# Optimization experiments

Hardware: AMD Instinct MI355X
Metric: run time of the kernel (lower is better)

The kernel has to match this reference:

```python
import jax, jax.numpy as jnp
import numpy as np
import math

B, S, E = 4, 2048, 1024


def setup_inputs() -> dict:
    key = jax.random.key(0)
    ks = jax.random.split(key, 9)
    x = jax.random.normal(ks[0], (B, S, E), dtype=jnp.float32)
    # causal boolean mask, broadcast over batch: True = keep
    mask = jnp.broadcast_to(jnp.tril(jnp.ones((S, S), dtype=bool)), (B, S, S))
    sc = 1.0 / math.sqrt(E)
    Wq = jax.random.normal(ks[1], (E, E), dtype=jnp.float32) * sc
    bq = jnp.zeros((E,), dtype=jnp.float32)
    Wk = jax.random.normal(ks[2], (E, E), dtype=jnp.float32) * sc
    bk = jnp.zeros((E,), dtype=jnp.float32)
    Wv = jax.random.normal(ks[3], (E, E), dtype=jnp.float32) * sc
    bv = jnp.zeros((E,), dtype=jnp.float32)
    gamma = jnp.ones((E,), dtype=jnp.float32)
    beta = jnp.zeros((E,), dtype=jnp.float32)
    return {"x": x, "mask": mask, "Wq": Wq, "bq": bq, "Wk": Wk, "bk": bk,
            "Wv": Wv, "bv": bv, "gamma": gamma, "beta": beta}


def reference(x, mask, Wq, bq, Wk, bk, Wv, bv, gamma, beta):
    E_ = x.shape[-1]
    q = jnp.einsum('bse,fe->bsf', x, Wq) + bq
    k = jnp.einsum('bse,fe->bsf', x, Wk) + bk
    v = jnp.einsum('bse,fe->bsf', x, Wv) + bv
    scores = jnp.einsum('bqe,bke->bqk', q, k) / jnp.sqrt(jnp.float32(E_))
    scores = jnp.where(mask, scores, -jnp.inf)
    probs = jax.nn.softmax(scores, axis=-1)
    attn = jnp.einsum('bqk,bke->bqe', probs, v)
    y = attn + x
    # LayerNorm over last dim, eps matches torch default 1e-5
    mu = jnp.mean(y, axis=-1, keepdims=True)
    var = jnp.mean(jnp.square(y - mu), axis=-1, keepdims=True)
    return (y - mu) / jnp.sqrt(var + 1e-5) * gamma + beta
```

## Files before the change

kernel.cpp:

```cpp
#include <hip/hip_runtime.h>
#include <hip/hip_bf16.h>
#include <stdint.h>

#define B_ 4
#define S_ 2048
#define E_ 1024
#define BS_ (B_*S_)

using bf16x8 = __attribute__((ext_vector_type(8))) __bf16;
using f32x4  = __attribute__((ext_vector_type(4))) float;

__constant__ int pv_mt[24] = {7,8,9,10,11,12,13,14,15,15,14,6,13,5,12,4,11,3,10,2,9,1,8,0};
__constant__ int pv_ck[24] = {0,0,0,0,0,0,0,0,0, 1, 1,0, 1,0, 1,0, 1,0, 1,0, 1,0, 1,0};

__device__ __forceinline__ unsigned short f2bf(float f) {
  unsigned int u = __float_as_uint(f);
  u += 0x7fffu + ((u >> 16) & 1u);
  return (unsigned short)(u >> 16);
}
__device__ __forceinline__ float bf2f(unsigned short h) {
  return __uint_as_float(((unsigned int)h) << 16);
}

__device__ __forceinline__ void gld16(const unsigned short* g, unsigned short* l) {
  __builtin_amdgcn_global_load_lds((__attribute__((address_space(1))) void*)(void*)g,
                                   (__attribute__((address_space(3))) void*)l, 16, 0, 0);
}

__global__ __launch_bounds__(256) void prep_all(
    const float* __restrict__ x,
    const float* __restrict__ Wq, const float* __restrict__ Wk, const float* __restrict__ Wv,
    const float* __restrict__ bq, const float* __restrict__ bk, const float* __restrict__ bv,
    unsigned short* __restrict__ xb, unsigned short* __restrict__ Wb, float* __restrict__ bb,
    float* __restrict__ lz) {
  const int i = blockIdx.x * 256 + threadIdx.x;
  const int nx4 = BS_ * E_ / 4, nw4 = E_ * E_ / 4;
  if (i < nx4) {
    const float4 v = ((const float4*)x)[i];
    ushort4 o;
    o.x = f2bf(v.x); o.y = f2bf(v.y); o.z = f2bf(v.z); o.w = f2bf(v.w);
    ((ushort4*)xb)[i] = o;
  } else if (i < nx4 + 3 * nw4) {
    const int j = i - nx4;
    const int m = j / nw4, jj = j - m * nw4;
    const float* src = (m == 0) ? Wq : (m == 1) ? Wk : Wv;
    const float4 v = ((const float4*)src)[jj];
    ushort4 o;
    o.x = f2bf(v.x); o.y = f2bf(v.y); o.z = f2bf(v.z); o.w = f2bf(v.w);
    ((ushort4*)Wb)[j] = o;
  } else {
    const int j = i - nx4 - 3 * nw4;
    if (j < 3 * E_) bb[j] = (j < E_) ? bq[j] : (j < 2 * E_) ? bk[j - E_] : bv[j - 2 * E_];
    else { const int k = j - 3 * E_; if (k < BS_) lz[k] = 0.f; }
  }
}

template<int EPI>
__device__ __forceinline__ void gemm_body(
    const unsigned short* __restrict__ A, const unsigned short* __restrict__ Bm,
    float* __restrict__ Cf,
    unsigned short* __restrict__ Cb, unsigned short* __restrict__ VtOut,
    const float* __restrict__ bias,
    int K, int lda, int ldb, int ldc,
    long sA, long sB, long sC, float scale)
{
  constexpr int BM = 128, BN = 128, BK = 64;
  __shared__ __align__(16) unsigned short As[BM * BK];
  __shared__ __align__(16) unsigned short Bs[BN * BK];

  int mt, nt, ck = 0, bz;
  if (EPI == 1) {
    const int sig = (blockIdx.x & 7) * 68 + (blockIdx.x >> 3);
    bz = sig / 136;
    const int rem = sig - bz * 136;
    const int M = (rem >= 78) ? 3 : (rem >= 36) ? 2 : (rem >= 10) ? 1 : 0;
    const int cumM = (M == 3) ? 78 : (M == 2) ? 36 : (M == 1) ? 10 : 0;
    const int inner = rem - cumM;
    if (inner < 16 * M) {
      const int N = inner >> 4, t2 = inner & 15;
      mt = 4 * M + (t2 >> 2); nt = 4 * N + (t2 & 3);
    } else {
      const int t2 = inner - 16 * M;
      const int ml = (t2 >= 6) ? 3 : (t2 >= 3) ? 2 : (t2 >= 1) ? 1 : 0;
      const int nl = t2 - (ml * (ml + 1)) / 2;
      mt = 4 * M + ml; nt = 4 * M + nl;
    }
  } else if (EPI == 2) {
    mt = pv_mt[blockIdx.y]; ck = pv_ck[blockIdx.y]; nt = blockIdx.x; bz = blockIdx.z;
  } else {
    const int nwg = gridDim.x * gridDim.y;
    const int bid = blockIdx.y * gridDim.x + blockIdx.x;
    const int swz = (bid & 7) * (nwg >> 3) + (bid >> 3);
    mt = swz / gridDim.x; nt = swz - mt * gridDim.x; bz = blockIdx.z;
  }
  A  += sA * bz;
  Bm += sB * bz;
  const int m0 = mt * BM, n0 = nt * BN;
  const int k0s  = (EPI == 2 && ck) ? 1024 : 0;
  const int kend = (EPI == 2) ? (ck ? m0 + BM : min(1024, m0 + BM)) : K;

  const int t = threadIdx.x;
  const int lane = t & 63, wave = t >> 6;
  const int wr = wave >> 1, wc = wave & 1;
  const int q = lane >> 4, r = lane & 15;

  const int srow   = lane >> 3;
  const int schunk = (lane & 7) ^ srow;
  const long ga0 = (long)(m0 + wave * 32 + srow) * lda + schunk * 8;
  const long gb0 = (long)(n0 + wave * 32 + srow) * ldb + schunk * 8;

  f32x4 acc[4][4] = {};

  for (int k0 = k0s; k0 < kend; k0 += BK) {
#pragma unroll
    for (int s = 0; s < 4; ++s) {
      gld16(A  + ga0 + (long)s * 8 * lda + k0, &As[(wave * 32 + s * 8) * 64]);
      gld16(Bm + gb0 + (long)s * 8 * ldb + k0, &Bs[(wave * 32 + s * 8) * 64]);
    }
    __syncthreads();
#pragma unroll
    for (int kk = 0; kk < BK; kk += 32) {
      bf16x8 af[4], bfr[4];
      const int cq = (kk >> 3) + q;
#pragma unroll
      for (int i = 0; i < 4; ++i) {
        const int row = wr * 64 + i * 16 + r;
        af[i] = *(const bf16x8*)&As[(row * 8 + (cq ^ (r & 7))) * 8];
      }
#pragma unroll
      for (int j = 0; j < 4; ++j) {
        const int row = wc * 64 + j * 16 + r;
        bfr[j] = *(const bf16x8*)&Bs[(row * 8 + (cq ^ (r & 7))) * 8];
      }
#pragma unroll
      for (int i = 0; i < 4; ++i)
#pragma unroll
        for (int j = 0; j < 4; ++j)
          acc[i][j] = __builtin_amdgcn_mfma_f32_16x16x32_bf16(af[i], bfr[j], acc[i][j], 0, 0, 0);
    }
    __syncthreads();
  }

  if (EPI == 0) {
    if (n0 < 2 * E_) {
#pragma unroll
    for (int i = 0; i < 4; ++i)
#pragma unroll
      for (int j = 0; j < 4; ++j) {
        const int col = n0 + wc * 64 + j * 16 + r;
        const float bia = bias[col];
#pragma unroll
        for (int e = 0; e < 4; ++e) {
          const int rowg = m0 + wr * 64 + i * 16 + q * 4 + e;
          Cb[(long)rowg * ldc + col] = f2bf(acc[i][j][e] + bia);
        }
      }
    } else {
      unsigned short* scr = As + wave * 2048;
      const int bb = m0 >> 11;
      const int sbase = (m0 & (S_ - 1)) + wr * 64;
#pragma unroll
      for (int j = 0; j < 4; ++j) {
        const int e_base = n0 - 2 * E_ + wc * 64 + j * 16;
        const float bj = bias[n0 + wc * 64 + j * 16 + r];
#pragma unroll
        for (int i = 0; i < 4; ++i) {
          const int c = 2 * i + (q >> 1);
          const int slot = c ^ (r & 7);
          ushort4 o;
          o.x = f2bf(acc[i][j][0] + bj);
          o.y = f2bf(acc[i][j][1] + bj);
          o.z = f2bf(acc[i][j][2] + bj);
          o.w = f2bf(acc[i][j][3] + bj);
          *(ushort4*)&scr[r * 72 + slot * 8 + (q & 1) * 4] = o;
        }
#pragma unroll
        for (int it = 0; it < 2; ++it) {
          const int er = it * 8 + (lane >> 3);
          const int w = lane & 7;
          const bf16x8 vv = *(const bf16x8*)&scr[er * 72 + w * 8];
          const int so = (w ^ (er & 7)) * 8;
          *(bf16x8*)&VtOut[((long)bb * E_ + e_base + er) * S_ + sbase + so] = vv;
        }
      }
    }
  } else if (EPI == 1) {
    Cb += sC * bz;
    float* lv = Cf + (long)bz * S_;
#pragma unroll
    for (int i = 0; i < 4; ++i) {
      float rs[4] = {0.f, 0.f, 0.f, 0.f};
#pragma unroll
      for (int j = 0; j < 4; ++j) {
        const int col = n0 + wc * 64 + j * 16 + r;
#pragma unroll
        for (int e = 0; e < 4; ++e) {
          const int rowg = m0 + wr * 64 + i * 16 + q * 4 + e;
          float p = 0.f;
          if (col <= rowg) p = __expf(fminf(acc[i][j][e] * scale, 60.f));
          Cb[(long)rowg * ldc + col] = f2bf(p);
          rs[e] += p;
        }
      }
#pragma unroll
      for (int e = 0; e < 4; ++e) {
        float s = rs[e];
        s += __shfl_xor(s, 1); s += __shfl_xor(s, 2);
        s += __shfl_xor(s, 4); s += __shfl_xor(s, 8);
        if (r == 0) atomicAdd(&lv[m0 + wr * 64 + i * 16 + q * 4 + e], s);
      }
    }
  } else {
    const float* lv = Cf + (long)bz * S_;
    unsigned short* dst = (ck ? VtOut : Cb) + sC * bz;
#pragma unroll
    for (int i = 0; i < 4; ++i) {
      const int rb = m0 + wr * 64 + i * 16 + q * 4;
      const float4 l4 = *(const float4*)&lv[rb];
      const float r0 = 1.f / l4.x, r1 = 1.f / l4.y, r2 = 1.f / l4.z, r3 = 1.f / l4.w;
#pragma unroll
      for (int j = 0; j < 4; ++j) {
        const int col = n0 + wc * 64 + j * 16 + r;
        dst[(long)(rb + 0) * ldc + col] = f2bf(acc[i][j][0] * r0);
        dst[(long)(rb + 1) * ldc + col] = f2bf(acc[i][j][1] * r1);
        dst[(long)(rb + 2) * ldc + col] = f2bf(acc[i][j][2] * r2);
        dst[(long)(rb + 3) * ldc + col] = f2bf(acc[i][j][3] * r3);
      }
    }
  }
}

__global__ __launch_bounds__(256, 4) void gemm_qkv(
    const unsigned short* A, const unsigned short* Bm, float* Cf,
    unsigned short* Cb, unsigned short* VtOut, const float* bias,
    int K, int lda, int ldb, int ldc, long sA, long sB, long sC, float scale) {
  gemm_body<0>(A, Bm, Cf, Cb, VtOut, bias, K, lda, ldb, ldc, sA, sB, sC, scale);
}
__global__ __launch_bounds__(256, 4) void gemm_sc(
    const unsigned short* A, const unsigned short* Bm, float* Cf,
    unsigned short* Cb, unsigned short* VtOut, const float* bias,
    int K, int lda, int ldb, int ldc, long sA, long sB, long sC, float scale) {
  gemm_body<1>(A, Bm, Cf, Cb, VtOut, bias, K, lda, ldb, ldc, sA, sB, sC, scale);
}
__global__ __launch_bounds__(256, 4) void gemm_pv(
    const unsigned short* A, const unsigned short* Bm, float* Cf,
    unsigned short* Cb, unsigned short* VtOut, const float* bias,
    int K, int lda, int ldb, int ldc, long sA, long sB, long sC, float scale) {
  gemm_body<2>(A, Bm, Cf, Cb, VtOut, bias, K, lda, ldb, ldc, sA, sB, sC, scale);
}

__global__ __launch_bounds__(256) void residual_ln(
    const unsigned short* __restrict__ attn, const unsigned short* __restrict__ attn2,
    const unsigned short* __restrict__ xb,
    const float* __restrict__ gamma, const float* __restrict__ beta,
    float* __restrict__ out) {
  __shared__ float rs[4], rs2[4];
  const long row = blockIdx.x;
  const int t = threadIdx.x;
  const int lane = t & 63, wave = t >> 6;
  const ushort4 a  = ((const ushort4*)(attn + row * E_))[t];
  const ushort4 xv = ((const ushort4*)(xb + row * E_))[t];
  ushort4 b2 = make_ushort4(0, 0, 0, 0);
  if ((row & (S_ - 1)) >= 1024) b2 = ((const ushort4*)(attn2 + row * E_))[t];
  const float y0 = bf2f(a.x) + bf2f(b2.x) + bf2f(xv.x);
  const float y1 = bf2f(a.y) + bf2f(b2.y) + bf2f(xv.y);
  const float y2 = bf2f(a.z) + bf2f(b2.z) + bf2f(xv.z);
  const float y3 = bf2f(a.w) + bf2f(b2.w) + bf2f(xv.w);
  float s  = y0 + y1 + y2 + y3;
  float s2 = y0 * y0 + y1 * y1 + y2 * y2 + y3 * y3;
#pragma unroll
  for (int o = 32; o; o >>= 1) { s += __shfl_xor(s, o); s2 += __shfl_xor(s2, o); }
  if (lane == 0) { rs[wave] = s; rs2[wave] = s2; }
  __syncthreads();
  s  = rs[0] + rs[1] + rs[2] + rs[3];
  s2 = rs2[0] + rs2[1] + rs2[2] + rs2[3];
  const float mu  = s * (1.0f / E_);
  const float var = s2 * (1.0f / E_) - mu * mu;
  const float inv = rsqrtf(var + 1e-5f);
  const float4 g  = ((const float4*)gamma)[t];
  const float4 be = ((const float4*)beta)[t];
  float4 o;
  o.x = (y0 - mu) * inv * g.x + be.x;
  o.y = (y1 - mu) * inv * g.y + be.y;
  o.z = (y2 - mu) * inv * g.z + be.z;
  o.w = (y3 - mu) * inv * g.w + be.w;
  ((float4*)(out + row * E_))[t] = o;
}

extern "C" void kernel_launch(void* const* d_in, const int* in_sizes, int n_in,
                              void* d_out, int out_size, void* d_ws, size_t ws_size,
                              hipStream_t stream) {
  const float* x  = (const float*)d_in[0];
  const float* Wq = (const float*)d_in[2];
  const float* bq = (const float*)d_in[3];
  const float* Wk = (const float*)d_in[4];
  const float* bk = (const float*)d_in[5];
  const float* Wv = (const float*)d_in[6];
  const float* bv = (const float*)d_in[7];
  const float* gamma = (const float*)d_in[8];
  const float* beta  = (const float*)d_in[9];
  float* out = (float*)d_out;

  char* ws = (char*)d_ws;
  size_t off = 0;
  auto alloc = [&](size_t bytes) { char* p = ws + off; off += (bytes + 255) & ~(size_t)255; return p; };
  unsigned short* xb    = (unsigned short*)alloc((size_t)BS_ * E_ * 2);
  unsigned short* Wqkvb = (unsigned short*)alloc((size_t)3 * E_ * E_ * 2);
  float*          bqkv  = (float*)alloc((size_t)3 * E_ * 4);
  unsigned short* Cqkv  = (unsigned short*)alloc((size_t)BS_ * 2 * E_ * 2);
  unsigned short* Vt    = (unsigned short*)alloc((size_t)BS_ * E_ * 2);
  unsigned short* Sc    = (unsigned short*)alloc((size_t)B_ * S_ * S_ * 2);
  float*          lrow  = (float*)alloc((size_t)BS_ * 4);
  unsigned short* attn  = (unsigned short*)Cqkv;
  unsigned short* attn2 = (unsigned short*)Cqkv + (size_t)BS_ * E_;

  const int nprep = BS_ * E_ / 4 + 3 * E_ * E_ / 4 + 3 * E_ + BS_;
  prep_all<<<dim3((nprep + 255) / 256), 256, 0, stream>>>(x, Wq, Wk, Wv, bq, bk, bv,
                                                          xb, Wqkvb, bqkv, lrow);

  dim3 g1(3 * E_ / 128, BS_ / 128, 1);
  gemm_qkv<<<g1, 256, 0, stream>>>(xb, Wqkvb, nullptr, Cqkv, Vt, bqkv,
                                   E_, E_, E_, 2 * E_, 0, 0, 0, 1.f);

  gemm_sc<<<dim3(544), 256, 0, stream>>>(Cqkv, Cqkv + E_, lrow, Sc, nullptr, nullptr,
                                         E_, 2 * E_, 2 * E_, S_,
                                         (long)S_ * 2 * E_, (long)S_ * 2 * E_, (long)S_ * S_,
                                         0.03125f);

  dim3 g3(E_ / 128, 24, B_);
  gemm_pv<<<g3, 256, 0, stream>>>(Sc, Vt, lrow, attn, attn2, nullptr,
                                  S_, S_, S_, E_,
                                  (long)S_ * S_, (long)S_ * E_, (long)S_ * E_, 1.f);

  residual_ln<<<dim3(BS_), 256, 0, stream>>>(attn, attn2, xb, gamma, beta, out);
}
```

Measured before the change: 270.3 us.

## Replace causal score GEMM with 64x128 tile kernel over lower-triangular tiles

Replaces the 128x128 causal score GEMM, with its grouped triangular tile mapping, by a dedicated kernel using 64x128 tiles. Only tiles on or below the diagonal are launched, 1088 blocks instead of 544. Smaller M tiles cut the wasted masked work on diagonal tiles and give finer load balance. The cost is lower A/B reuse per block, more global loads, more atomics on the row sums, and a simple single-buffered K loop with a serial while loop to map each block to its tile.

```diff
diff --git a/kernel.cpp b/kernel.cpp
--- a/kernel.cpp
+++ b/kernel.cpp
@@ -69,23 +69,7 @@
   __shared__ __align__(16) unsigned short Bs[BN * BK];
 
   int mt, nt, ck = 0, bz;
-  if (EPI == 1) {
-    const int sig = (blockIdx.x & 7) * 68 + (blockIdx.x >> 3);
-    bz = sig / 136;
-    const int rem = sig - bz * 136;
-    const int M = (rem >= 78) ? 3 : (rem >= 36) ? 2 : (rem >= 10) ? 1 : 0;
-    const int cumM = (M == 3) ? 78 : (M == 2) ? 36 : (M == 1) ? 10 : 0;
-    const int inner = rem - cumM;
-    if (inner < 16 * M) {
-      const int N = inner >> 4, t2 = inner & 15;
-      mt = 4 * M + (t2 >> 2); nt = 4 * N + (t2 & 3);
-    } else {
-      const int t2 = inner - 16 * M;
-      const int ml = (t2 >= 6) ? 3 : (t2 >= 3) ? 2 : (t2 >= 1) ? 1 : 0;
-      const int nl = t2 - (ml * (ml + 1)) / 2;
-      mt = 4 * M + ml; nt = 4 * M + nl;
-    }
-  } else if (EPI == 2) {
+  if (EPI == 2) {
     mt = pv_mt[blockIdx.y]; ck = pv_ck[blockIdx.y]; nt = blockIdx.x; bz = blockIdx.z;
   } else {
     const int nwg = gridDim.x * gridDim.y;
@@ -184,32 +168,6 @@
         }
       }
     }
-  } else if (EPI == 1) {
-    Cb += sC * bz;
-    float* lv = Cf + (long)bz * S_;
-#pragma unroll
-    for (int i = 0; i < 4; ++i) {
-      float rs[4] = {0.f, 0.f, 0.f, 0.f};
-#pragma unroll
-      for (int j = 0; j < 4; ++j) {
-        const int col = n0 + wc * 64 + j * 16 + r;
-#pragma unroll
-        for (int e = 0; e < 4; ++e) {
-          const int rowg = m0 + wr * 64 + i * 16 + q * 4 + e;
-          float p = 0.f;
-          if (col <= rowg) p = __expf(fminf(acc[i][j][e] * scale, 60.f));
-          Cb[(long)rowg * ldc + col] = f2bf(p);
-          rs[e] += p;
-        }
-      }
-#pragma unroll
-      for (int e = 0; e < 4; ++e) {
-        float s = rs[e];
-        s += __shfl_xor(s, 1); s += __shfl_xor(s, 2);
-        s += __shfl_xor(s, 4); s += __shfl_xor(s, 8);
-        if (r == 0) atomicAdd(&lv[m0 + wr * 64 + i * 16 + q * 4 + e], s);
-      }
-    }
   } else {
     const float* lv = Cf + (long)bz * S_;
     unsigned short* dst = (ck ? VtOut : Cb) + sC * bz;
@@ -236,17 +194,100 @@
     int K, int lda, int ldb, int ldc, long sA, long sB, long sC, float scale) {
   gemm_body<0>(A, Bm, Cf, Cb, VtOut, bias, K, lda, ldb, ldc, sA, sB, sC, scale);
 }
-__global__ __launch_bounds__(256, 4) void gemm_sc(
-    const unsigned short* A, const unsigned short* Bm, float* Cf,
-    unsigned short* Cb, unsigned short* VtOut, const float* bias,
-    int K, int lda, int ldb, int ldc, long sA, long sB, long sC, float scale) {
-  gemm_body<1>(A, Bm, Cf, Cb, VtOut, bias, K, lda, ldb, ldc, sA, sB, sC, scale);
-}
 __global__ __launch_bounds__(256, 4) void gemm_pv(
     const unsigned short* A, const unsigned short* Bm, float* Cf,
     unsigned short* Cb, unsigned short* VtOut, const float* bias,
     int K, int lda, int ldb, int ldc, long sA, long sB, long sC, float scale) {
   gemm_body<2>(A, Bm, Cf, Cb, VtOut, bias, K, lda, ldb, ldc, sA, sB, sC, scale);
+}
+
+__global__ __launch_bounds__(256, 4) void gemm_sc64(
+    const unsigned short* __restrict__ A, const unsigned short* __restrict__ Bm,
+    float* __restrict__ Cf, unsigned short* __restrict__ Cb,
+    int lda, int ldb, int ldc, long sA, long sB, long sC, float scale)
+{
+  constexpr int BK = 64;
+  __shared__ __align__(16) unsigned short As[64 * BK];
+  __shared__ __align__(16) unsigned short Bs[128 * BK];
+
+  const int sig = (blockIdx.x & 7) * 136 + (blockIdx.x >> 3);
+  const int bz  = sig / 272;
+  const int rem = sig - bz * 272;
+  int mt = 0, c = 0;
+  while (c + (mt / 2 + 1) <= rem) { c += mt / 2 + 1; ++mt; }
+  const int nt = rem - c;
+  const int m0 = mt * 64, n0 = nt * 128;
+
+  const unsigned short* Ab = A + sA * bz;
+  const unsigned short* Bb = Bm + sB * bz;
+
+  const int t = threadIdx.x;
+  const int lane = t & 63, wave = t >> 6;
+  const int q = lane >> 4, r = lane & 15;
+
+  const int srow   = lane >> 3;
+  const int schunk = (lane & 7) ^ srow;
+  const long ga0 = (long)(m0 + wave * 16 + srow) * lda + schunk * 8;
+  const long gb0 = (long)(n0 + wave * 32 + srow) * ldb + schunk * 8;
+
+  f32x4 acc[4][2] = {};
+
+  for (int k0 = 0; k0 < E_; k0 += BK) {
+#pragma unroll
+    for (int s = 0; s < 2; ++s)
+      gld16(Ab + ga0 + (long)s * 8 * lda + k0, &As[(wave * 16 + s * 8) * 64]);
+#pragma unroll
+    for (int s = 0; s < 4; ++s)
+      gld16(Bb + gb0 + (long)s * 8 * ldb + k0, &Bs[(wave * 32 + s * 8) * 64]);
+    __syncthreads();
+#pragma unroll
+    for (int kk = 0; kk < BK; kk += 32) {
+      bf16x8 af[4], bfr[2];
+      const int cq = (kk >> 3) + q;
+#pragma unroll
+      for (int i = 0; i < 4; ++i) {
+        const int row = i * 16 + r;
+        af[i] = *(const bf16x8*)&As[(row * 8 + (cq ^ (r & 7))) * 8];
+      }
+#pragma unroll
+      for (int j = 0; j < 2; ++j) {
+        const int row = wave * 32 + j * 16 + r;
+        bfr[j] = *(const bf16x8*)&Bs[(row * 8 + (cq ^ (r & 7))) * 8];
+      }
+#pragma unroll
+      for (int i = 0; i < 4; ++i)
+#pragma unroll
+        for (int j = 0; j < 2; ++j)
+          acc[i][j] = __builtin_amdgcn_mfma_f32_16x16x32_bf16(af[i], bfr[j], acc[i][j], 0, 0, 0);
+    }
+    __syncthreads();
+  }
+
+  unsigned short* Cbz = Cb + sC * bz;
+  float* lv = Cf + (long)bz * S_;
+#pragma unroll
+  for (int i = 0; i < 4; ++i) {
+    float rs[4] = {0.f, 0.f, 0.f, 0.f};
+    const int rowg0 = m0 + i * 16 + q * 4;
+#pragma unroll
+    for (int j = 0; j < 2; ++j) {
+      const int col = n0 + wave * 32 + j * 16 + r;
+#pragma unroll
+      for (int e = 0; e < 4; ++e) {
+        float p = 0.f;
+        if (col <= rowg0 + e) p = __expf(fminf(acc[i][j][e] * scale, 60.f));
+        Cbz[(long)(rowg0 + e) * ldc + col] = f2bf(p);
+        rs[e] += p;
+      }
+    }
+#pragma unroll
+    for (int e = 0; e < 4; ++e) {
+      float s = rs[e];
+      s += __shfl_xor(s, 1); s += __shfl_xor(s, 2);
+      s += __shfl_xor(s, 4); s += __shfl_xor(s, 8);
+      if (r == 0) atomicAdd(&lv[rowg0 + e], s);
+    }
+  }
 }
 
 __global__ __launch_bounds__(256) void residual_ln(
@@ -322,10 +363,10 @@
   gemm_qkv<<<g1, 256, 0, stream>>>(xb, Wqkvb, nullptr, Cqkv, Vt, bqkv,
                                    E_, E_, E_, 2 * E_, 0, 0, 0, 1.f);
 
-  gemm_sc<<<dim3(544), 256, 0, stream>>>(Cqkv, Cqkv + E_, lrow, Sc, nullptr, nullptr,
-                                         E_, 2 * E_, 2 * E_, S_,
-                                         (long)S_ * 2 * E_, (long)S_ * 2 * E_, (long)S_ * S_,
-                                         0.03125f);
+  gemm_sc64<<<dim3(1088), 256, 0, stream>>>(Cqkv, Cqkv + E_, lrow, Sc,
+                                            2 * E_, 2 * E_, S_,
+                                            (long)S_ * 2 * E_, (long)S_ * 2 * E_,
+                                            (long)S_ * S_, 0.03125f);
 
   dim3 g3(E_ / 128, 24, B_);
   gemm_pv<<<g3, 256, 0, stream>>>(Sc, Vt, lrow, attn, attn2, nullptr,
```

After: 284.7 us. 1.05x slower.
